# Kernel tuning notes

Measured on AMD Instinct MI355X. Metric: run time of the kernel, lower is better.

## Reference

```python
import jax, jax.numpy as jnp
import numpy as np

TOP_K = 2
NORM_TOPK_PROB = True


def setup_inputs() -> dict:
    key = jax.random.key(0)
    k1, k2, k3 = jax.random.split(key, 3)
    B, S, H, E = 4, 2048, 2048, 8
    hidden_states = jax.random.normal(k1, (B, S, H), dtype=jnp.float32)
    gate_w = jax.random.normal(k2, (E, H), dtype=jnp.float32) * 0.02   # nn.Linear weight [E, H]
    expert_w = jax.random.normal(k3, (E, H, H), dtype=jnp.float32) * 0.02  # per-expert Linear weight [H_out, H_in]
    return {"hidden_states": hidden_states, "gate_w": gate_w, "expert_w": expert_w}


def reference(hidden_states, gate_w, expert_w):
    B, S, H = hidden_states.shape
    E = gate_w.shape[0]
    x = hidden_states.reshape(-1, H)                      # [T, H], T = B*S
    T = x.shape[0]

    router_logits = x @ gate_w.T                          # [T, E]
    probs = jax.nn.softmax(router_logits.astype(jnp.float32), axis=-1)
    top_w, top_i = jax.lax.top_k(probs, TOP_K)            # [T, K]
    if NORM_TOPK_PROB:
        top_w = top_w / jnp.sum(top_w, axis=-1, keepdims=True)
    top_w = top_w.astype(x.dtype)

    # dense [T, E] combine weights (scatter of top-k weights)
    w_full = jnp.zeros((T, E), dtype=x.dtype).at[jnp.arange(T)[:, None], top_i].add(top_w)

    # expert_i(x) = x @ W_i.T  (bias-free Linear)
    expert_out = jnp.einsum('th,eoh->eto', x, expert_w)   # [E, T, H]
    out = jnp.einsum('te,eto->to', w_full, expert_out)    # [T, H]

    return out.reshape(B, S, H), router_logits.reshape(B, S, E)
```

## Files before the change

### kernel.cpp

```cpp
#include <hip/hip_runtime.h>
#include <stdint.h>

#define T_TOK 8192
#define HDIM  2048
#define NEXP  8
#define TILE  128
#define BK    64
#define RTOK  32

typedef __bf16 bf16x8 __attribute__((ext_vector_type(8)));
typedef float  f32x4  __attribute__((ext_vector_type(4)));
typedef unsigned short u16;
typedef u16    u16x8  __attribute__((ext_vector_type(8)));

typedef const __attribute__((address_space(1))) void* gptr_t;
typedef __attribute__((address_space(3))) void* lptr_t;

static __device__ __forceinline__ u16 f2bf(float f) {
    union { float f; unsigned u; } v; v.f = f;
    unsigned u = v.u;
    u = (u + 0x7FFFu + ((u >> 16) & 1u)) >> 16;
    return (u16)u;
}

__global__ __launch_bounds__(256) void cvt_kernel(const float* __restrict__ in,
                                                  u16* __restrict__ out, int n8) {
    int i = blockIdx.x * 256 + threadIdx.x;
    if (i >= n8) return;
    const float4* p = (const float4*)in + (size_t)i * 2;
    float4 a = p[0], b = p[1];
    u16x8 r;
    r[0] = f2bf(a.x); r[1] = f2bf(a.y); r[2] = f2bf(a.z); r[3] = f2bf(a.w);
    r[4] = f2bf(b.x); r[5] = f2bf(b.y); r[6] = f2bf(b.z); r[7] = f2bf(b.w);
    ((u16x8*)out)[i] = r;
}

__global__ __launch_bounds__(256) void router_kernel(const float* __restrict__ x,
                                                     const float* __restrict__ gw,
                                                     u16* __restrict__ xb,
                                                     float* __restrict__ logits_out,
                                                     int* __restrict__ cnt,
                                                     int* __restrict__ rows,
                                                     float* __restrict__ wts) {
    __shared__ int   lcnt[NEXP];
    __shared__ int   lbase[NEXP];
    __shared__ int   lrows[NEXP][RTOK];
    __shared__ float lwtsS[NEXP][RTOK];

    int tid  = threadIdx.x;
    int lane = tid & 63;
    int wave = tid >> 6;
    if (tid < NEXP) lcnt[tid] = 0;
    __syncthreads();

    int t0 = blockIdx.x * RTOK + wave * 8;
    const float4* g4 = (const float4*)gw;

    float acc[8][NEXP] = {};
    #pragma unroll
    for (int i = 0; i < HDIM / 4 / 64; i++) {
        int idx = lane + i * 64;
        float4 gv[NEXP];
        #pragma unroll
        for (int e = 0; e < NEXP; e++) gv[e] = g4[e * (HDIM / 4) + idx];
        #pragma unroll
        for (int tk = 0; tk < 8; tk++) {
            int t = t0 + tk;
            float4 xv = ((const float4*)(x + (size_t)t * HDIM))[idx];
            ushort4 h;
            h.x = f2bf(xv.x); h.y = f2bf(xv.y); h.z = f2bf(xv.z); h.w = f2bf(xv.w);
            ((ushort4*)(xb + (size_t)t * HDIM))[idx] = h;
            #pragma unroll
            for (int e = 0; e < NEXP; e++)
                acc[tk][e] += xv.x * gv[e].x + xv.y * gv[e].y +
                              xv.z * gv[e].z + xv.w * gv[e].w;
        }
    }
    #pragma unroll
    for (int tk = 0; tk < 8; tk++)
        #pragma unroll
        for (int e = 0; e < NEXP; e++)
            #pragma unroll
            for (int off = 32; off > 0; off >>= 1)
                acc[tk][e] += __shfl_xor(acc[tk][e], off, 64);

    if (lane == 0) {
        #pragma unroll
        for (int tk = 0; tk < 8; tk++) {
            int t = t0 + tk;
            #pragma unroll
            for (int e = 0; e < NEXP; e++) logits_out[(size_t)t * NEXP + e] = acc[tk][e];
            int e0 = 0;
            #pragma unroll
            for (int e = 1; e < NEXP; e++) if (acc[tk][e] > acc[tk][e0]) e0 = e;
            int e1 = (e0 == 0) ? 1 : 0;
            #pragma unroll
            for (int e = 0; e < NEXP; e++)
                if (e != e0 && acc[tk][e] > acc[tk][e1]) e1 = e;
            float w0 = 1.0f / (1.0f + expf(acc[tk][e1] - acc[tk][e0]));
            int p0 = atomicAdd(&lcnt[e0], 1);
            lrows[e0][p0] = t; lwtsS[e0][p0] = w0;
            int p1 = atomicAdd(&lcnt[e1], 1);
            lrows[e1][p1] = t; lwtsS[e1][p1] = 1.0f - w0;
        }
    }
    __syncthreads();
    if (tid < NEXP) lbase[tid] = atomicAdd(&cnt[tid], lcnt[tid]);
    __syncthreads();
    int e = tid >> 5, j = tid & 31;
    if (j < lcnt[e]) {
        int b = lbase[e] + j;
        rows[e * T_TOK + b] = lrows[e][j];
        wts[e * T_TOK + b]  = lwtsS[e][j];
    }
}

__global__ __launch_bounds__(256) void moe_gemm(const u16* __restrict__ xb,
                                                const u16* __restrict__ wb,
                                                const int* __restrict__ cnt,
                                                const int* __restrict__ rows,
                                                const float* __restrict__ wts,
                                                float* __restrict__ out) {
    int p  = blockIdx.x;
    int xc = p & 7;
    int q  = p >> 3;
    int rt = q & 63;
    int g  = (q >> 6) * 8 + xc;
    int e  = g >> 4;
    int nb = (g & 15) * TILE;

    int count = cnt[e];
    int rowBase = rt * TILE;
    if (rowBase >= count) return;

    const u16*   W     = wb  + (size_t)e * HDIM * HDIM;
    const int*   rlist = rows + e * T_TOK;
    const float* wlist = wts  + e * T_TOK;

    __shared__ u16 As[2][TILE * BK];
    __shared__ u16 Bs[2][TILE * BK];

    int tid  = threadIdx.x;
    int lane = tid & 63;
    int wave = tid >> 6;
    int wr = wave >> 1, wc = wave & 1;

    const u16* a_src[4];
    const u16* b_src[4];
    #pragma unroll
    for (int pp = 0; pp < 4; pp++) {
        int row  = (tid >> 3) + pp * 32;
        int clog = (tid & 7) ^ (row & 7);
        int tok  = rlist[min(rowBase + row, count - 1)];
        a_src[pp] = xb + (size_t)tok * HDIM + clog * 8;
        b_src[pp] = W + (size_t)(nb + row) * HDIM + clog * 8;
    }
    int wslot = (tid & ~63);

    auto stage = [&](u16* A_lds, u16* B_lds, int kb) {
        #pragma unroll
        for (int pp = 0; pp < 4; pp++) {
            __builtin_amdgcn_global_load_lds((gptr_t)(a_src[pp] + kb),
                                             (lptr_t)(A_lds + (pp * 256 + wslot) * 8),
                                             16, 0, 0);
            __builtin_amdgcn_global_load_lds((gptr_t)(b_src[pp] + kb),
                                             (lptr_t)(B_lds + (pp * 256 + wslot) * 8),
                                             16, 0, 0);
        }
    };

    int lrow = lane & 15;
    int kq   = lane >> 4;
    int mloc[4], nloc[4];
    #pragma unroll
    for (int i = 0; i < 4; i++) {
        mloc[i] = wr * 64 + i * 16 + lrow;
        nloc[i] = wc * 64 + i * 16 + lrow;
    }

    f32x4 acc[4][4] = {};

    auto compute = [&](const u16* A_lds, const u16* B_lds) {
        #pragma unroll
        for (int s = 0; s < 2; s++) {
            int chunk = s * 4 + kq;
            bf16x8 a[4], b[4];
            #pragma unroll
            for (int i = 0; i < 4; i++) {
                int aslot = (mloc[i] << 3) | (chunk ^ (mloc[i] & 7));
                int bslot = (nloc[i] << 3) | (chunk ^ (nloc[i] & 7));
                a[i] = *(const bf16x8*)(A_lds + aslot * 8);
                b[i] = *(const bf16x8*)(B_lds + bslot * 8);
            }
            #pragma unroll
            for (int mt = 0; mt < 4; mt++)
                #pragma unroll
                for (int nt = 0; nt < 4; nt++)
                    acc[mt][nt] = __builtin_amdgcn_mfma_f32_16x16x32_bf16(
                                      a[mt], b[nt], acc[mt][nt], 0, 0, 0);
        }
    };

    stage(As[0], Bs[0], 0);
    stage(As[1], Bs[1], BK);

    for (int kb = 0; kb < HDIM - 2 * BK; kb += 2 * BK) {
        asm volatile("s_waitcnt vmcnt(8)" ::: "memory");
        __builtin_amdgcn_sched_barrier(0);
        __builtin_amdgcn_s_barrier();
        compute(As[0], Bs[0]);
        __builtin_amdgcn_sched_barrier(0);
        __builtin_amdgcn_s_barrier();
        stage(As[0], Bs[0], kb + 2 * BK);

        asm volatile("s_waitcnt vmcnt(8)" ::: "memory");
        __builtin_amdgcn_sched_barrier(0);
        __builtin_amdgcn_s_barrier();
        compute(As[1], Bs[1]);
        __builtin_amdgcn_sched_barrier(0);
        __builtin_amdgcn_s_barrier();
        stage(As[1], Bs[1], kb + 3 * BK);
    }
    asm volatile("s_waitcnt vmcnt(8)" ::: "memory");
    __builtin_amdgcn_sched_barrier(0);
    __builtin_amdgcn_s_barrier();
    compute(As[0], Bs[0]);
    asm volatile("s_waitcnt vmcnt(0)" ::: "memory");
    __builtin_amdgcn_sched_barrier(0);
    __builtin_amdgcn_s_barrier();
    compute(As[1], Bs[1]);

    int srow = (lane >> 4) * 4;
    #pragma unroll
    for (int mt = 0; mt < 4; mt++) {
        #pragma unroll
        for (int r = 0; r < 4; r++) {
            int row = rowBase + wr * 64 + mt * 16 + srow + r;
            if (row < count) {
                int   tok = rlist[row];
                float wgt = wlist[row];
                #pragma unroll
                for (int nt = 0; nt < 4; nt++) {
                    int col = nb + wc * 64 + nt * 16 + lrow;
                    atomicAdd(out + (size_t)tok * HDIM + col, wgt * acc[mt][nt][r]);
                }
            }
        }
    }
}

extern "C" void kernel_launch(void* const* d_in, const int* in_sizes, int n_in,
                              void* d_out, int out_size, void* d_ws, size_t ws_size,
                              hipStream_t stream) {
    const float* x  = (const float*)d_in[0];
    const float* gw = (const float*)d_in[1];
    const float* ew = (const float*)d_in[2];
    float* out    = (float*)d_out;
    float* logits = out + (size_t)T_TOK * HDIM;

    char* ws = (char*)d_ws;
    int*   cnt  = (int*)ws;
    int*   rows = (int*)(ws + 1024);
    float* wts  = (float*)(ws + 1024 + 262144);
    u16*   xb   = (u16*)(ws + 1024 + 2 * 262144);
    u16*   wb   = xb + (size_t)T_TOK * HDIM;

    hipMemsetAsync(d_out, 0, (size_t)T_TOK * HDIM * sizeof(float), stream);
    hipMemsetAsync(cnt, 0, NEXP * sizeof(int), stream);

    int nw8 = NEXP * HDIM * HDIM / 8;
    cvt_kernel<<<(nw8 + 255) / 256, 256, 0, stream>>>(ew, wb, nw8);

    router_kernel<<<T_TOK / RTOK, 256, 0, stream>>>(x, gw, xb, logits, cnt, rows, wts);

    moe_gemm<<<NEXP * 64 * 16, 256, 0, stream>>>(xb, wb, cnt, rows, wts, out);
}
```

Measured before the change: 595.1 us.

## Replace atomic scatter-add with per-slot bf16 buffer and combine kernel

The GEMM epilogue now writes each routed token-slot's weighted expert output as bf16 into a dedicated slot buffer (two slots per token) instead of doing fp32 atomicAdd into the output. A new combine kernel sums the two slot rows per token into the fp32 output, which also removes the need to zero the output beforehand. This avoids atomic contention and the output memset, at the cost of an extra intermediate buffer round trip, scattered 2-byte stores, and bf16 rounding of partial results.

```diff
diff --git a/kernel.cpp b/kernel.cpp
--- a/kernel.cpp
+++ b/kernel.cpp
@@ -99,9 +99,9 @@
                 if (e != e0 && acc[tk][e] > acc[tk][e1]) e1 = e;
             float w0 = 1.0f / (1.0f + expf(acc[tk][e1] - acc[tk][e0]));
             int p0 = atomicAdd(&lcnt[e0], 1);
-            lrows[e0][p0] = t; lwtsS[e0][p0] = w0;
+            lrows[e0][p0] = t * 2;     lwtsS[e0][p0] = w0;
             int p1 = atomicAdd(&lcnt[e1], 1);
-            lrows[e1][p1] = t; lwtsS[e1][p1] = 1.0f - w0;
+            lrows[e1][p1] = t * 2 + 1; lwtsS[e1][p1] = 1.0f - w0;
         }
     }
     __syncthreads();
@@ -120,7 +120,7 @@
                                                 const int* __restrict__ cnt,
                                                 const int* __restrict__ rows,
                                                 const float* __restrict__ wts,
-                                                float* __restrict__ out) {
+                                                u16* __restrict__ cbuf) {
     int p  = blockIdx.x;
     int xc = p & 7;
     int q  = p >> 3;
@@ -151,7 +151,7 @@
     for (int pp = 0; pp < 4; pp++) {
         int row  = (tid >> 3) + pp * 32;
         int clog = (tid & 7) ^ (row & 7);
-        int tok  = rlist[min(rowBase + row, count - 1)];
+        int tok  = rlist[min(rowBase + row, count - 1)] >> 1;
         a_src[pp] = xb + (size_t)tok * HDIM + clog * 8;
         b_src[pp] = W + (size_t)(nb + row) * HDIM + clog * 8;
     }
@@ -237,16 +237,36 @@
         for (int r = 0; r < 4; r++) {
             int row = rowBase + wr * 64 + mt * 16 + srow + r;
             if (row < count) {
-                int   tok = rlist[row];
-                float wgt = wlist[row];
+                int   slot = rlist[row];
+                float wgt  = wlist[row];
+                u16* crow = cbuf + (size_t)slot * HDIM;
                 #pragma unroll
                 for (int nt = 0; nt < 4; nt++) {
                     int col = nb + wc * 64 + nt * 16 + lrow;
-                    atomicAdd(out + (size_t)tok * HDIM + col, wgt * acc[mt][nt][r]);
+                    crow[col] = f2bf(wgt * acc[mt][nt][r]);
                 }
             }
         }
     }
+}
+
+__global__ __launch_bounds__(256) void combine_kernel(const u16* __restrict__ cbuf,
+                                                      float* __restrict__ out) {
+    int t  = blockIdx.x;
+    int c8 = threadIdx.x;
+    u16x8 a = ((const u16x8*)(cbuf + (size_t)(t * 2)     * HDIM))[c8];
+    u16x8 b = ((const u16x8*)(cbuf + (size_t)(t * 2 + 1) * HDIM))[c8];
+    float4 o[2];
+    #pragma unroll
+    for (int j = 0; j < 8; j++) {
+        union { unsigned u; float f; } va, vb;
+        va.u = (unsigned)a[j] << 16;
+        vb.u = (unsigned)b[j] << 16;
+        ((float*)o)[j] = va.f + vb.f;
+    }
+    float4* op = (float4*)(out + (size_t)t * HDIM + c8 * 8);
+    op[0] = o[0];
+    op[1] = o[1];
 }
 
 extern "C" void kernel_launch(void* const* d_in, const int* in_sizes, int n_in,
@@ -264,8 +284,8 @@
     float* wts  = (float*)(ws + 1024 + 262144);
     u16*   xb   = (u16*)(ws + 1024 + 2 * 262144);
     u16*   wb   = xb + (size_t)T_TOK * HDIM;
-
-    hipMemsetAsync(d_out, 0, (size_t)T_TOK * HDIM * sizeof(float), stream);
+    u16*   cbuf = wb + (size_t)NEXP * HDIM * HDIM;
+
     hipMemsetAsync(cnt, 0, NEXP * sizeof(int), stream);
 
     int nw8 = NEXP * HDIM * HDIM / 8;
@@ -273,5 +293,7 @@
 
     router_kernel<<<T_TOK / RTOK, 256, 0, stream>>>(x, gw, xb, logits, cnt, rows, wts);
 
-    moe_gemm<<<NEXP * 64 * 16, 256, 0, stream>>>(xb, wb, cnt, rows, wts, out);
-}
+    moe_gemm<<<NEXP * 64 * 16, 256, 0, stream>>>(xb, wb, cnt, rows, wts, cbuf);
+
+    combine_kernel<<<T_TOK, 256, 0, stream>>>(cbuf, out);
+}
```

Result: faster. 560.9 us (-5.8%).
